# Performance work log

Measured on AMD Instinct MI355X. Metric: run time of the kernel, lower is better.

Reference implementation:

```python
import jax, jax.numpy as jnp
import numpy as np

D_MODEL = 1024
N_HEADS = 16
D_HEAD = D_MODEL // N_HEADS


def setup_inputs() -> dict:
    key = jax.random.key(0)
    ks = jax.random.split(key, 6)
    query = jax.random.normal(ks[0], (2, 2048, D_MODEL), dtype=jnp.float32)
    context = jax.random.normal(ks[1], (2, 4096, D_MODEL), dtype=jnp.float32)
    s = 1.0 / np.sqrt(D_MODEL)
    Wq = jax.random.normal(ks[2], (D_MODEL, D_MODEL), dtype=jnp.float32) * s
    Wk = jax.random.normal(ks[3], (D_MODEL, D_MODEL), dtype=jnp.float32) * s
    Wv = jax.random.normal(ks[4], (D_MODEL, D_MODEL), dtype=jnp.float32) * s
    Wo = jax.random.normal(ks[5], (D_MODEL, D_MODEL), dtype=jnp.float32) * s
    return {"query": query, "context": context, "Wq": Wq, "Wk": Wk, "Wv": Wv, "Wo": Wo}


def reference(query, context, Wq, Wk, Wv, Wo):
    B, T_q, D = query.shape
    T_c = context.shape[1]
    # nn.Linear(bias=False): y = x @ W.T
    Q = (query @ Wq.T).reshape(B, T_q, N_HEADS, D_HEAD)
    K = (context @ Wk.T).reshape(B, T_c, N_HEADS, D_HEAD)
    V = (context @ Wv.T).reshape(B, T_c, N_HEADS, D_HEAD)
    scale = jnp.sqrt(jnp.asarray(D_HEAD, dtype=query.dtype))
    # non-causal cross-attention; chunking in the original is mathematically
    # identical to the full softmax attention below
    scores = jnp.einsum('bqhd,bkhd->bhqk', Q, K) / scale
    attn = jax.nn.softmax(scores, axis=-1)
    out = jnp.einsum('bhqk,bkhd->bqhd', attn, V).reshape(B, T_q, D)
    return out @ Wo.T
```

## Files before the change

kernel.cpp:

```cpp
#include <hip/hip_runtime.h>

typedef __attribute__((__ext_vector_type__(4))) float f32x4;
typedef __attribute__((__ext_vector_type__(16))) float f32x16;
typedef __attribute__((__ext_vector_type__(8))) __bf16 bf16x8;
typedef __attribute__((__ext_vector_type__(4))) unsigned int u32x4;

#define AS1 __attribute__((address_space(1)))
#define AS3 __attribute__((address_space(3)))

__device__ __forceinline__ unsigned short f2bf(float f) {
  unsigned int u = __float_as_uint(f);
  u += 0x7FFFu + ((u >> 16) & 1u);
  return (unsigned short)(u >> 16);
}
__device__ __forceinline__ unsigned int packtrunc(float lo, float hi) {
  return (__float_as_uint(hi) & 0xFFFF0000u) | (__float_as_uint(lo) >> 16);
}

__global__ void cast_all(const float* __restrict__ q, const float* __restrict__ c,
                         const float* __restrict__ wq, const float* __restrict__ wk,
                         const float* __restrict__ wv, const float* __restrict__ wo,
                         unsigned short* __restrict__ qb, unsigned short* __restrict__ cb,
                         unsigned short* __restrict__ wqb, unsigned short* __restrict__ wkb,
                         unsigned short* __restrict__ wvb, unsigned short* __restrict__ wob) {
  const int blk = blockIdx.x;
  const float* s; unsigned short* d; int off;
  if (blk < 4096)        { s = q;  d = qb;  off = blk; }
  else if (blk < 12288)  { s = c;  d = cb;  off = blk - 4096; }
  else if (blk < 13312)  { s = wq; d = wqb; off = blk - 12288; }
  else if (blk < 14336)  { s = wk; d = wkb; off = blk - 13312; }
  else if (blk < 15360)  { s = wv; d = wvb; off = blk - 14336; }
  else                   { s = wo; d = wob; off = blk - 15360; }
  const long i = ((long)off * 256 + threadIdx.x) * 4;
  float4 v = *reinterpret_cast<const float4*>(s + i);
  ushort4 o;
  o.x = f2bf(v.x); o.y = f2bf(v.y); o.z = f2bf(v.z); o.w = f2bf(v.w);
  *reinterpret_cast<ushort4*>(d + i) = o;
}

__device__ __forceinline__ void gemm_core(const unsigned short* __restrict__ A,
                                          const unsigned short* __restrict__ Bt,
                                          unsigned short* As, unsigned short* Bs,
                                          int m0, int n0, f32x4 acc[4][4]) {
  const int tid = threadIdx.x, lane = tid & 63, wid = tid >> 6;
  const int fr = lane & 15, fg = lane >> 4;
  const int wr = wid >> 1, wc = wid & 1;
  const int srow = wid * 16 + (lane >> 2);
  const int scol = (lane & 3) * 8;
  const unsigned short* a0 = A + (long)(m0 + srow) * 1024 + scol;
  const unsigned short* b0 = Bt + (long)(n0 + srow) * 1024 + scol;

  for (int k0 = 0; k0 < 1024; k0 += 32) {
    __builtin_amdgcn_global_load_lds((const AS1 void*)(a0 + k0),
                                     (AS3 void*)(As + wid * 512), 16, 0, 0);
    __builtin_amdgcn_global_load_lds((const AS1 void*)(a0 + 64 * 1024 + k0),
                                     (AS3 void*)(As + 2048 + wid * 512), 16, 0, 0);
    __builtin_amdgcn_global_load_lds((const AS1 void*)(b0 + k0),
                                     (AS3 void*)(Bs + wid * 512), 16, 0, 0);
    __builtin_amdgcn_global_load_lds((const AS1 void*)(b0 + 64 * 1024 + k0),
                                     (AS3 void*)(Bs + 2048 + wid * 512), 16, 0, 0);
    __syncthreads();
    bf16x8 af[4], bfr[4];
#pragma unroll
    for (int m = 0; m < 4; ++m)
      af[m] = *reinterpret_cast<const bf16x8*>(&As[(wr * 64 + m * 16 + fr) * 32 + fg * 8]);
#pragma unroll
    for (int n = 0; n < 4; ++n)
      bfr[n] = *reinterpret_cast<const bf16x8*>(&Bs[(wc * 64 + n * 16 + fr) * 32 + fg * 8]);
#pragma unroll
    for (int m = 0; m < 4; ++m)
#pragma unroll
      for (int n = 0; n < 4; ++n)
        acc[m][n] = __builtin_amdgcn_mfma_f32_16x16x32_bf16(af[m], bfr[n], acc[m][n], 0, 0, 0);
    __syncthreads();
  }
}

__global__ __launch_bounds__(256) void proj_fused(const unsigned short* __restrict__ qb,
                                                  const unsigned short* __restrict__ cb,
                                                  const unsigned short* __restrict__ wqb,
                                                  const unsigned short* __restrict__ wkb,
                                                  const unsigned short* __restrict__ wvb,
                                                  unsigned short* __restrict__ Qb,
                                                  unsigned short* __restrict__ Kb,
                                                  unsigned short* __restrict__ Vt) {
  const int bid = blockIdx.x;
  const unsigned short *A, *Bt; unsigned short* C; int mode, loc;
  if (bid < 256)      { A = qb; Bt = wqb; C = Qb; mode = 0; loc = bid; }
  else if (bid < 768) { A = cb; Bt = wkb; C = Kb; mode = 0; loc = bid - 256; }
  else                { A = cb; Bt = wvb; C = Vt; mode = 2; loc = bid - 768; }
  const int m0 = (loc >> 3) << 7, n0 = (loc & 7) << 7;

  __shared__ __align__(16) unsigned short As[128 * 32];
  __shared__ __align__(16) unsigned short Bs[128 * 32];
  f32x4 acc[4][4];
#pragma unroll
  for (int m = 0; m < 4; ++m)
#pragma unroll
    for (int n = 0; n < 4; ++n) acc[m][n] = {0.f, 0.f, 0.f, 0.f};

  gemm_core(A, Bt, As, Bs, m0, n0, acc);

  const int lane = threadIdx.x & 63, wid = threadIdx.x >> 6;
  const int fr = lane & 15, fg = lane >> 4, wr = wid >> 1, wc = wid & 1;
  if (mode == 0) {
#pragma unroll
    for (int m = 0; m < 4; ++m) {
      const int row = m0 + wr * 64 + m * 16 + fg * 4;
#pragma unroll
      for (int n = 0; n < 4; ++n) {
        const int col = n0 + wc * 64 + n * 16 + fr;
#pragma unroll
        for (int r = 0; r < 4; ++r)
          C[(long)(row + r) * 1024 + col] = f2bf(acc[m][n][r]);
      }
    }
  } else {
#pragma unroll
    for (int m = 0; m < 4; ++m) {
      const int row = m0 + wr * 64 + m * 16 + fg * 4;
      const int bb = row >> 12, t = row & 4095;
#pragma unroll
      for (int n = 0; n < 4; ++n) {
        const int col = n0 + wc * 64 + n * 16 + fr;
        ushort4 o;
        o.x = f2bf(acc[m][n][0]); o.y = f2bf(acc[m][n][1]);
        o.z = f2bf(acc[m][n][2]); o.w = f2bf(acc[m][n][3]);
        *reinterpret_cast<ushort4*>(&C[((long)(bb * 1024 + col)) * 4096 + t]) = o;
      }
    }
  }
}

__global__ __launch_bounds__(256) void gemm_o(const unsigned short* __restrict__ A,
                                              const unsigned short* __restrict__ Bt,
                                              float* __restrict__ C) {
  const int m0 = ((int)blockIdx.x >> 3) << 7, n0 = ((int)blockIdx.x & 7) << 7;
  __shared__ __align__(16) unsigned short As[128 * 32];
  __shared__ __align__(16) unsigned short Bs[128 * 32];
  f32x4 acc[4][4];
#pragma unroll
  for (int m = 0; m < 4; ++m)
#pragma unroll
    for (int n = 0; n < 4; ++n) acc[m][n] = {0.f, 0.f, 0.f, 0.f};
  gemm_core(A, Bt, As, Bs, m0, n0, acc);
  const int lane = threadIdx.x & 63, wid = threadIdx.x >> 6;
  const int fr = lane & 15, fg = lane >> 4, wr = wid >> 1, wc = wid & 1;
#pragma unroll
  for (int m = 0; m < 4; ++m) {
    const int row = m0 + wr * 64 + m * 16 + fg * 4;
#pragma unroll
    for (int n = 0; n < 4; ++n) {
      const int col = n0 + wc * 64 + n * 16 + fr;
#pragma unroll
      for (int r = 0; r < 4; ++r)
        C[(long)(row + r) * 1024 + col] = acc[m][n][r];
    }
  }
}

#define SC 0.18033688011112042f
#define MSC 5.7707801635558535f

__global__ __launch_bounds__(256, 2) void flash_attn(const unsigned short* __restrict__ Q,
                                                     const unsigned short* __restrict__ Kb,
                                                     const unsigned short* __restrict__ Vt,
                                                     unsigned short* __restrict__ AO) {
  const int tid = threadIdx.x, lane = tid & 63, wid = tid >> 6;
  const int qt = (int)blockIdx.x & 15;
  const int h = ((int)blockIdx.x >> 4) & 15;
  const int b = (int)blockIdx.x >> 8;
  const int q0 = qt * 128;
  const int l = lane & 31, hi = lane >> 5, l7 = l & 7;

  __shared__ __align__(16) unsigned short Ks[2][4096];
  __shared__ __align__(16) unsigned short Vs[2][4096];

  bf16x8 qf[4];
#pragma unroll
  for (int dk = 0; dk < 4; ++dk)
    qf[dk] = *reinterpret_cast<const bf16x8*>(
        &Q[(long)(b * 2048 + q0 + wid * 32 + l) * 1024 + h * 64 + dk * 16 + hi * 8]);

  f32x16 oacc[2];
  oacc[0] = (f32x16)(0.f); oacc[1] = (f32x16)(0.f);
  float lsum = 0.f;

  const int lr = lane >> 3;
  const int swc = (lane & 7) ^ lr;
  const unsigned short* ks0 = Kb + (long)(b * 4096 + wid * 16 + lr) * 1024 + h * 64 + swc * 8;
  const unsigned short* vs0 = Vt + (long)((b * 16 + h) * 64 + wid * 16 + lr) * 4096 + swc * 8;

#define STAGE(buf, t)                                                                         \
  {                                                                                           \
    const long ko = (long)(t) * 65536;                                                        \
    const int vo = (t) * 64;                                                                  \
    __builtin_amdgcn_global_load_lds((const AS1 void*)(ks0 + ko),                             \
                                     (AS3 void*)(&Ks[buf][wid * 1024]), 16, 0, 0);            \
    __builtin_amdgcn_global_load_lds((const AS1 void*)(ks0 + ko + 8 * 1024),                  \
                                     (AS3 void*)(&Ks[buf][wid * 1024 + 512]), 16, 0, 0);      \
    __builtin_amdgcn_global_load_lds((const AS1 void*)(vs0 + vo),                             \
                                     (AS3 void*)(&Vs[buf][wid * 1024]), 16, 0, 0);            \
    __builtin_amdgcn_global_load_lds((const AS1 void*)(vs0 + vo + 8 * 4096),                  \
                                     (AS3 void*)(&Vs[buf][wid * 1024 + 512]), 16, 0, 0);      \
  }

  STAGE(0, 0);

  for (int t = 0; t < 64; ++t) {
    const int cur = t & 1;
    if (t < 63) {
      STAGE(cur ^ 1, t + 1);
      asm volatile("s_waitcnt vmcnt(4)" ::: "memory");
    } else {
      asm volatile("s_waitcnt vmcnt(0)" ::: "memory");
    }
    __builtin_amdgcn_s_barrier();
    __builtin_amdgcn_sched_barrier(0);

    f32x16 s2[2];
    s2[0] = (f32x16)(0.f); s2[1] = (f32x16)(0.f);
#pragma unroll
    for (int kvb = 0; kvb < 2; ++kvb) {
#pragma unroll
      for (int dk = 0; dk < 4; ++dk) {
        const int r = kvb * 32 + l;
        bf16x8 kf = *reinterpret_cast<const bf16x8*>(
            &Ks[cur][r * 64 + (((dk * 2 + hi) ^ l7) * 8)]);
        s2[kvb] = __builtin_amdgcn_mfma_f32_32x32x16_bf16(kf, qf[dk], s2[kvb], 0, 0, 0);
      }
    }

    bf16x8 pA[4];
#pragma unroll
    for (int kvb = 0; kvb < 2; ++kvb) {
      float p[16];
      float ps = 0.f;
#pragma unroll
      for (int r = 0; r < 16; ++r) {
        p[r] = __builtin_amdgcn_exp2f(fmaf(s2[kvb][r], SC, -MSC));
        ps += p[r];
      }
      lsum += ps;
      unsigned int pk[8];
#pragma unroll
      for (int i = 0; i < 8; ++i) pk[i] = packtrunc(p[2 * i], p[2 * i + 1]);
      asm("v_permlane32_swap_b32 %0, %1" : "+v"(pk[0]), "+v"(pk[2]));
      asm("v_permlane32_swap_b32 %0, %1" : "+v"(pk[1]), "+v"(pk[3]));
      asm("v_permlane32_swap_b32 %0, %1" : "+v"(pk[4]), "+v"(pk[6]));
      asm("v_permlane32_swap_b32 %0, %1" : "+v"(pk[5]), "+v"(pk[7]));
      u32x4 w0 = {pk[0], pk[1], pk[2], pk[3]};
      u32x4 w1 = {pk[4], pk[5], pk[6], pk[7]};
      pA[kvb * 2] = __builtin_bit_cast(bf16x8, w0);
      pA[kvb * 2 + 1] = __builtin_bit_cast(bf16x8, w1);
    }

#pragma unroll
    for (int dblk = 0; dblk < 2; ++dblk) {
      const int r = dblk * 32 + l;
#pragma unroll
      for (int seg = 0; seg < 4; ++seg) {
        bf16x8 vf = *reinterpret_cast<const bf16x8*>(
            &Vs[cur][r * 64 + (((seg * 2 + hi) ^ l7) * 8)]);
        oacc[dblk] = __builtin_amdgcn_mfma_f32_32x32x16_bf16(pA[seg], vf, oacc[dblk], 0, 0, 0);
      }
    }
    __builtin_amdgcn_s_barrier();
  }

  lsum += __shfl_xor(lsum, 32);
  const float inv = 1.0f / lsum;
#pragma unroll
  for (int reg = 0; reg < 16; ++reg) {
    const int qrow = (reg & 3) + 8 * (reg >> 2) + 4 * hi;
    const float ivr = __shfl(inv, qrow, 64);
    const long rbase = (long)(b * 2048 + q0 + wid * 32 + qrow) * 1024 + h * 64;
    AO[rbase + l] = f2bf(oacc[0][reg] * ivr);
    AO[rbase + 32 + l] = f2bf(oacc[1][reg] * ivr);
  }
}

extern "C" void kernel_launch(void* const* d_in, const int* in_sizes, int n_in,
                              void* d_out, int out_size, void* d_ws, size_t ws_size,
                              hipStream_t stream) {
  const float* query = (const float*)d_in[0];
  const float* context = (const float*)d_in[1];
  const float* Wq = (const float*)d_in[2];
  const float* Wk = (const float*)d_in[3];
  const float* Wv = (const float*)d_in[4];
  const float* Wo = (const float*)d_in[5];

  char* ws = (char*)d_ws;
  unsigned short* qb = (unsigned short*)(ws);
  unsigned short* cb = (unsigned short*)(ws + 8388608);
  unsigned short* wqb = (unsigned short*)(ws + 25165824);
  unsigned short* wkb = (unsigned short*)(ws + 27262976);
  unsigned short* wvb = (unsigned short*)(ws + 29360128);
  unsigned short* wob = (unsigned short*)(ws + 31457280);
  unsigned short* Qb = (unsigned short*)(ws + 33554432);
  unsigned short* Kb = (unsigned short*)(ws + 41943040);
  unsigned short* Vt = (unsigned short*)(ws + 58720256);
  unsigned short* AO = qb;

  cast_all<<<16384, 256, 0, stream>>>(query, context, Wq, Wk, Wv, Wo,
                                      qb, cb, wqb, wkb, wvb, wob);
  proj_fused<<<1280, 256, 0, stream>>>(qb, cb, wqb, wkb, wvb, Qb, Kb, Vt);
  flash_attn<<<512, 256, 0, stream>>>(Qb, Kb, Vt, AO);
  gemm_o<<<256, 256, 0, stream>>>(AO, wob, (float*)d_out);
}
```

Baseline: 217.3 us.

## Split attention KV range across two blocks and add a combine kernel

Each attention block now handles half of the key/value sequence, doubling the grid from 512 to 1024 blocks. Each block writes a normalized partial output plus its row sums to scratch. A new combine kernel merges the two halves using weights derived from those row sums. Launch bounds rise to 4 blocks per CU. The aim is better occupancy and CU fill on the attention stage, at the cost of an extra kernel launch and extra memory traffic for the partial outputs.

```diff
diff --git a/kernel.cpp b/kernel.cpp
--- a/kernel.cpp
+++ b/kernel.cpp
@@ -3,6 +3,7 @@
 typedef __attribute__((__ext_vector_type__(4))) float f32x4;
 typedef __attribute__((__ext_vector_type__(16))) float f32x16;
 typedef __attribute__((__ext_vector_type__(8))) __bf16 bf16x8;
+typedef __attribute__((__ext_vector_type__(8))) unsigned short u16x8;
 typedef __attribute__((__ext_vector_type__(4))) unsigned int u32x4;
 
 #define AS1 __attribute__((address_space(1)))
@@ -12,6 +13,9 @@
   unsigned int u = __float_as_uint(f);
   u += 0x7FFFu + ((u >> 16) & 1u);
   return (unsigned short)(u >> 16);
+}
+__device__ __forceinline__ float bf2f(unsigned short u) {
+  return __uint_as_float((unsigned int)u << 16);
 }
 __device__ __forceinline__ unsigned int packtrunc(float lo, float hi) {
   return (__float_as_uint(hi) & 0xFFFF0000u) | (__float_as_uint(lo) >> 16);
@@ -162,14 +166,17 @@
 #define SC 0.18033688011112042f
 #define MSC 5.7707801635558535f
 
-__global__ __launch_bounds__(256, 2) void flash_attn(const unsigned short* __restrict__ Q,
+__global__ __launch_bounds__(256, 4) void flash_attn(const unsigned short* __restrict__ Q,
                                                      const unsigned short* __restrict__ Kb,
                                                      const unsigned short* __restrict__ Vt,
-                                                     unsigned short* __restrict__ AO) {
+                                                     unsigned short* __restrict__ Op,
+                                                     float* __restrict__ Lp) {
   const int tid = threadIdx.x, lane = tid & 63, wid = tid >> 6;
-  const int qt = (int)blockIdx.x & 15;
-  const int h = ((int)blockIdx.x >> 4) & 15;
-  const int b = (int)blockIdx.x >> 8;
+  const int blk = (int)blockIdx.x;
+  const int kvh = blk & 1;
+  const int qt = (blk >> 1) & 15;
+  const int h = (blk >> 5) & 15;
+  const int b = blk >> 9;
   const int q0 = qt * 128;
   const int l = lane & 31, hi = lane >> 5, l7 = l & 7;
 
@@ -188,8 +195,10 @@
 
   const int lr = lane >> 3;
   const int swc = (lane & 7) ^ lr;
-  const unsigned short* ks0 = Kb + (long)(b * 4096 + wid * 16 + lr) * 1024 + h * 64 + swc * 8;
-  const unsigned short* vs0 = Vt + (long)((b * 16 + h) * 64 + wid * 16 + lr) * 4096 + swc * 8;
+  const unsigned short* ks0 =
+      Kb + (long)(b * 4096 + kvh * 2048 + wid * 16 + lr) * 1024 + h * 64 + swc * 8;
+  const unsigned short* vs0 =
+      Vt + (long)((b * 16 + h) * 64 + wid * 16 + lr) * 4096 + kvh * 2048 + swc * 8;
 
 #define STAGE(buf, t)                                                                         \
   {                                                                                           \
@@ -207,9 +216,9 @@
 
   STAGE(0, 0);
 
-  for (int t = 0; t < 64; ++t) {
+  for (int t = 0; t < 32; ++t) {
     const int cur = t & 1;
-    if (t < 63) {
+    if (t < 31) {
       STAGE(cur ^ 1, t + 1);
       asm volatile("s_waitcnt vmcnt(4)" ::: "memory");
     } else {
@@ -270,14 +279,36 @@
 
   lsum += __shfl_xor(lsum, 32);
   const float inv = 1.0f / lsum;
+  if (hi == 0)
+    Lp[kvh * 65536 + (b * 2048 + q0 + wid * 32 + l) * 16 + h] = lsum;
+  unsigned short* Oh = Op + (long)kvh * 4194304;
 #pragma unroll
   for (int reg = 0; reg < 16; ++reg) {
     const int qrow = (reg & 3) + 8 * (reg >> 2) + 4 * hi;
     const float ivr = __shfl(inv, qrow, 64);
     const long rbase = (long)(b * 2048 + q0 + wid * 32 + qrow) * 1024 + h * 64;
-    AO[rbase + l] = f2bf(oacc[0][reg] * ivr);
-    AO[rbase + 32 + l] = f2bf(oacc[1][reg] * ivr);
-  }
+    Oh[rbase + l] = f2bf(oacc[0][reg] * ivr);
+    Oh[rbase + 32 + l] = f2bf(oacc[1][reg] * ivr);
+  }
+}
+
+__global__ void combine(const unsigned short* __restrict__ Op,
+                        const float* __restrict__ Lp,
+                        unsigned short* __restrict__ AO) {
+  const long i = ((long)blockIdx.x * 256 + threadIdx.x) * 8;
+  const int row = (int)(i >> 10);
+  const int h = ((int)(i >> 6)) & 15;
+  const float l0 = Lp[row * 16 + h];
+  const float l1 = Lp[65536 + row * 16 + h];
+  const float inv = 1.0f / (l0 + l1);
+  const float w0 = l0 * inv, w1 = l1 * inv;
+  u16x8 a = *reinterpret_cast<const u16x8*>(Op + i);
+  u16x8 bq = *reinterpret_cast<const u16x8*>(Op + 4194304 + i);
+  u16x8 o;
+#pragma unroll
+  for (int j = 0; j < 8; ++j)
+    o[j] = f2bf(bf2f(a[j]) * w0 + bf2f(bq[j]) * w1);
+  *reinterpret_cast<u16x8*>(AO + i) = o;
 }
 
 extern "C" void kernel_launch(void* const* d_in, const int* in_sizes, int n_in,
@@ -300,11 +331,14 @@
   unsigned short* Qb = (unsigned short*)(ws + 33554432);
   unsigned short* Kb = (unsigned short*)(ws + 41943040);
   unsigned short* Vt = (unsigned short*)(ws + 58720256);
+  unsigned short* Op = (unsigned short*)(ws + 8388608);
+  float* Lp = (float*)(ws + 25165824);
   unsigned short* AO = qb;
 
   cast_all<<<16384, 256, 0, stream>>>(query, context, Wq, Wk, Wv, Wo,
                                       qb, cb, wqb, wkb, wvb, wob);
   proj_fused<<<1280, 256, 0, stream>>>(qb, cb, wqb, wkb, wvb, Qb, Kb, Vt);
-  flash_attn<<<512, 256, 0, stream>>>(Qb, Kb, Vt, AO);
+  flash_attn<<<1024, 256, 0, stream>>>(Qb, Kb, Vt, Op, Lp);
+  combine<<<2048, 256, 0, stream>>>(Op, Lp, AO);
   gemm_o<<<256, 256, 0, stream>>>(AO, wob, (float*)d_out);
 }
```

New measurement: 216.4 us. About the same (-0.4%).
